# Optimization experiments

Hardware: AMD Instinct MI355X
Metric: run time of the kernel (lower is better)

Reference implementation:

```python
import jax, jax.numpy as jnp
import numpy as np

EPS = 1e-12


def _phi(e):
    # e: [C, L] -> pairwise euclidean distances [C, C], diagonal zeroed
    sq = jnp.sum(e * e, axis=1)                      # [C]
    prod = e @ e.T                                   # [C, C]
    d2 = sq[:, None] + sq[None, :] - 2.0 * prod
    d = jnp.sqrt(jnp.clip(d2, EPS, None))
    C = e.shape[0]
    return d * (1.0 - jnp.eye(C, dtype=e.dtype))


def setup_inputs() -> dict:
    key = jax.random.key(0)
    k1, k2, k3 = jax.random.split(key, 3)
    N, C, L = 64, 512, 256
    le_student = jax.random.normal(k1, (N, C, L), dtype=jnp.float32)
    le_teacher = jax.random.normal(k2, (N, C, L), dtype=jnp.float32)
    targets = jax.random.randint(k3, (N, C), 0, 2, dtype=jnp.int32)
    return {"le_student": le_student, "le_teacher": le_teacher, "targets": targets}


def reference(le_student, le_teacher, targets):
    N, C, L = le_student.shape
    m = targets.astype(le_student.dtype)             # [N, C] 0/1 mask
    es = le_student * m[:, :, None]                  # zero out negative rows
    et = le_teacher * m[:, :, None]

    Ds = jax.vmap(_phi)(es)                          # [N, C, C]
    Dt = jax.vmap(_phi)(et)                          # [N, C, C]

    eye = jnp.eye(C, dtype=m.dtype)
    pm = m[:, :, None] * m[:, None, :]               # pairs of positive rows
    offdiag = pm * (1.0 - eye)                       # off-diagonal positive pairs

    npos = jnp.sum(m, axis=1)                        # [N]
    cnt = npos * (npos - 1.0)                        # entries with d > 0 in submatrix
    valid = npos > 1.0
    safe_cnt = jnp.maximum(cnt, 1.0)

    mean_s = jnp.sum(Ds * offdiag, axis=(1, 2)) / safe_cnt
    mean_t = jax.lax.stop_gradient(jnp.sum(Dt * offdiag, axis=(1, 2)) / safe_cnt)
    mean_s = jnp.where(valid, mean_s, 1.0)
    mean_t = jnp.where(valid, mean_t, 1.0)

    d = Ds / mean_s[:, None, None]
    td = jax.lax.stop_gradient(Dt / mean_t[:, None, None])

    diff = d - td
    adiff = jnp.abs(diff)
    huber = jnp.where(adiff < 1.0, 0.5 * diff * diff, adiff - 0.5)

    per = jnp.sum(huber * pm, axis=(1, 2)) / jnp.maximum(npos, 1.0)
    return jnp.sum(jnp.where(valid, per, 0.0))
```

## Files before the change

kernel.cpp:

```cpp
#include <hip/hip_runtime.h>
#include <hip/hip_bf16.h>
#include <hip/hip_fp16.h>
#include <math.h>

#define NB 64
#define CC 512
#define LL 256

typedef __attribute__((ext_vector_type(4))) float floatx4;
typedef __attribute__((ext_vector_type(8))) short short8;

static __device__ __forceinline__ unsigned f2bf2(float x, float y) {
    __hip_bfloat162 h = __float22bfloat162_rn(make_float2(x, y));
    union { __hip_bfloat162 h; unsigned u; } c; c.h = h;
    return c.u;
}
static __device__ __forceinline__ unsigned short f2h(float x) {
    __half h = __float2half_rn(x);
    union { __half h; unsigned short u; } c; c.h = h;
    return c.u;
}
static __device__ __forceinline__ float h2f(unsigned u) {
    union { unsigned short u; __half h; } c; c.u = (unsigned short)u;
    return __half2float(c.h);
}

__global__ __launch_bounds__(256) void prep_kernel(
    const int* __restrict__ targets,
    int* __restrict__ idx, int* __restrict__ npos,
    float* __restrict__ sumS, float* __restrict__ sumT, float* __restrict__ out)
{
    const int n = blockIdx.x, tid = threadIdx.x;
    __shared__ int s_cnt[8], s_off[8];
    const int w = tid >> 6, lane = tid & 63;
    const int* tg = targets + n * CC;
    const bool p0 = tg[tid] != 0;
    const bool p1 = tg[tid + 256] != 0;
    const unsigned long long m0 = __ballot(p0);
    const unsigned long long m1 = __ballot(p1);
    if (lane == 0) { s_cnt[w] = __popcll(m0); s_cnt[4 + w] = __popcll(m1); }
    __syncthreads();
    if (tid == 0) {
        int a = 0;
        for (int i = 0; i < 8; ++i) { s_off[i] = a; a += s_cnt[i]; }
        npos[n] = a;
        sumS[n] = 0.0f; sumT[n] = 0.0f;
        if (n == 0) out[0] = 0.0f;
    }
    __syncthreads();
    const unsigned long long below = (1ull << lane) - 1ull;
    if (p0) idx[n * CC + s_off[w] + __popcll(m0 & below)] = tid;
    if (p1) idx[n * CC + s_off[4 + w] + __popcll(m1 & below)] = tid + 256;
}

static __device__ __forceinline__ bool decode_tile(int t, int u, int& tI, int& tJ) {
    if (t >= (u * (u + 1)) >> 1) return false;
    tI = 0;
    while (t >= u - tI) { t -= u - tI; ++tI; }
    tJ = tI + t;
    return true;
}

__global__ __launch_bounds__(256) void dist_kernel(
    const float* __restrict__ S, const float* __restrict__ T,
    const int* __restrict__ idx, const int* __restrict__ npos,
    float* __restrict__ sumS, float* __restrict__ sumT,
    unsigned short* __restrict__ Ds, unsigned short* __restrict__ Dt)
{
    const int bx = blockIdx.x;
    const int n = bx & (NB - 1);
    const int q = bx >> 6;
    const int mat = q & 1, t = q >> 1;
    const int np = npos[n];
    if (np < 2) return;
    int tI, tJ;
    if (!decode_tile(t, (np + 63) >> 6, tI, tJ)) return;
    const bool diag = (tI == tJ);

    __shared__ __align__(16) unsigned short lds[2][2][64][40];
    __shared__ float s_norm[2][64];
    __shared__ float red[4];

    const int tid = threadIdx.x;
    const int w = tid >> 6, lane = tid & 63;

    const float* P = (mat ? T : S) + (size_t)n * CC * LL;
    unsigned short* Dout = (mat ? Dt : Ds) + (((size_t)t * NB + n) << 12);
    float* sumP = mat ? sumT : sumS;

    const int srow = w * 32 + (lane >> 1);
    const int half = lane & 1;
    const bool stager = diag ? (srow < 64) : true;
    const int ab = srow >> 6, rloc = srow & 63;
    const int gk = (ab ? tJ : tI) * 64 + rloc;
    const int row = idx[n * CC + ((gk < np) ? gk : 0)];
    const char* rp = (const char*)P + (size_t)row * (LL * 4) + half * 64;

    float4 pre[4];
    float nsum = 0.0f;
    if (stager) {
        #pragma unroll
        for (int i = 0; i < 4; ++i) pre[i] = *(const float4*)(rp + i * 16);
    }

    const int m16 = lane & 15, quad = lane >> 4;
    const int bufB = diag ? 0 : 1;
    const int wrow = w * 16;

    floatx4 acc[4];
    #pragma unroll
    for (int c = 0; c < 4; ++c) { acc[c][0] = 0; acc[c][1] = 0; acc[c][2] = 0; acc[c][3] = 0; }

    for (int kk = 0; kk < 8; ++kk) {
        const int pb = kk & 1;
        if (stager) {
            #pragma unroll
            for (int i = 0; i < 4; ++i)
                nsum += pre[i].x * pre[i].x + pre[i].y * pre[i].y +
                        pre[i].z * pre[i].z + pre[i].w * pre[i].w;
            unsigned short* dst = &lds[ab][pb][rloc][half * 16];
            *(uint2*)(dst + 0)  = make_uint2(f2bf2(pre[0].x, pre[0].y), f2bf2(pre[0].z, pre[0].w));
            *(uint2*)(dst + 4)  = make_uint2(f2bf2(pre[1].x, pre[1].y), f2bf2(pre[1].z, pre[1].w));
            *(uint2*)(dst + 8)  = make_uint2(f2bf2(pre[2].x, pre[2].y), f2bf2(pre[2].z, pre[2].w));
            *(uint2*)(dst + 12) = make_uint2(f2bf2(pre[3].x, pre[3].y), f2bf2(pre[3].z, pre[3].w));
        }
        __syncthreads();
        if (stager && kk < 7) {
            #pragma unroll
            for (int i = 0; i < 4; ++i)
                pre[i] = *(const float4*)(rp + (kk + 1) * 128 + i * 16);
        }
        const short8 a = *(const short8*)&lds[0][pb][wrow + m16][quad * 8];
        #pragma unroll
        for (int c = 0; c < 4; ++c) {
            const short8 b = *(const short8*)&lds[bufB][pb][c * 16 + m16][quad * 8];
            acc[c] = __builtin_amdgcn_mfma_f32_16x16x32_bf16(a, b, acc[c], 0, 0, 0);
        }
    }

    if (stager) {
        const float v = nsum + __shfl_xor(nsum, 1);
        if (half == 0) s_norm[ab][rloc] = v;
    }
    __syncthreads();

    float l0 = 0.0f;
    #pragma unroll
    for (int c = 0; c < 4; ++c) {
        const int colL = c * 16 + m16;
        const int gj = tJ * 64 + colL;
        const float nB = s_norm[bufB][colL];
        #pragma unroll
        for (int r = 0; r < 4; ++r) {
            const int rowL = wrow + quad * 4 + r;
            const int gi = tI * 64 + rowL;
            const float d = sqrtf(fmaxf(s_norm[0][rowL] + nB - 2.0f * acc[c][r], 1e-12f));
            if (gi < np && gj < np && gi != gj) l0 += d;
            Dout[rowL * 64 + colL] = f2h(d);
        }
    }

    #pragma unroll
    for (int o = 32; o; o >>= 1) l0 += __shfl_down(l0, o);
    if (lane == 0) red[w] = l0;
    __syncthreads();
    if (tid == 0) {
        const float wgt = diag ? 1.0f : 2.0f;
        atomicAdd(sumP + n, wgt * (red[0] + red[1] + red[2] + red[3]));
    }
}

__global__ __launch_bounds__(256) void huber_kernel(
    const unsigned short* __restrict__ Ds, const unsigned short* __restrict__ Dt,
    const int* __restrict__ npos,
    const float* __restrict__ sumS, const float* __restrict__ sumT,
    float* __restrict__ out)
{
    const int bx = blockIdx.x;
    const int n = bx & (NB - 1), t = bx >> 6;
    const int np = npos[n];
    if (np < 2) return;
    int tI, tJ;
    if (!decode_tile(t, (np + 63) >> 6, tI, tJ)) return;

    const float cnt = (float)np * (float)(np - 1);
    const float inv_ms = cnt / sumS[n];
    const float inv_mt = cnt / sumT[n];

    const size_t slot = ((size_t)t * NB + n) << 12;
    const uint4* ps = (const uint4*)(Ds + slot);
    const uint4* pt = (const uint4*)(Dt + slot);
    const int tid = threadIdx.x;

    float h = 0.0f;
    #pragma unroll
    for (int it = 0; it < 2; ++it) {
        const int g = it * 256 + tid;
        const uint4 a = ps[g];
        const uint4 b = pt[g];
        const unsigned aw[4] = { a.x, a.y, a.z, a.w };
        const unsigned bw[4] = { b.x, b.y, b.z, b.w };
        const int e0 = g * 8;
        #pragma unroll
        for (int k = 0; k < 8; ++k) {
            const int e = e0 + k;
            const int gi = tI * 64 + (e >> 6);
            const int gj = tJ * 64 + (e & 63);
            if (gi < np && gj < np && gi != gj) {
                const unsigned wa = aw[k >> 1], wb = bw[k >> 1];
                const float ds = h2f((k & 1) ? (wa >> 16) : (wa & 0xffffu));
                const float dt = h2f((k & 1) ? (wb >> 16) : (wb & 0xffffu));
                const float diff = ds * inv_ms - dt * inv_mt;
                const float ad = fabsf(diff);
                h += (ad < 1.0f) ? 0.5f * diff * diff : ad - 0.5f;
            }
        }
    }

    #pragma unroll
    for (int o = 32; o; o >>= 1) h += __shfl_down(h, o);
    __shared__ float red[4];
    const int w = tid >> 6, lane = tid & 63;
    if (lane == 0) red[w] = h;
    __syncthreads();
    if (tid == 0) {
        const float wgt = (tI == tJ) ? 1.0f : 2.0f;
        atomicAdd(out, wgt * (red[0] + red[1] + red[2] + red[3]) / (float)np);
    }
}

extern "C" void kernel_launch(void* const* d_in, const int* in_sizes, int n_in,
                              void* d_out, int out_size, void* d_ws, size_t ws_size,
                              hipStream_t stream) {
    const float* S = (const float*)d_in[0];
    const float* T = (const float*)d_in[1];
    const int* targets = (const int*)d_in[2];
    float* out = (float*)d_out;

    char* p = (char*)d_ws;
    int* idx = (int*)p;        p += (size_t)NB * CC * 4;
    int* npos = (int*)p;       p += NB * 4;
    float* sumS = (float*)p;   p += NB * 4;
    float* sumT = (float*)p;   p += NB * 4;
    p = (char*)(((size_t)p + 255) & ~(size_t)255);
    unsigned short* Ds = (unsigned short*)p;   p += (size_t)36 * NB * 4096 * 2;
    unsigned short* Dt = (unsigned short*)p;

    prep_kernel<<<NB, 256, 0, stream>>>(targets, idx, npos, sumS, sumT, out);
    dist_kernel<<<72 * NB, 256, 0, stream>>>(S, T, idx, npos, sumS, sumT, Ds, Dt);
    huber_kernel<<<36 * NB, 256, 0, stream>>>(Ds, Dt, npos, sumS, sumT, out);
}
```

Measured before the change: 124.8 us.

## Fuse Huber pass into distance kernel via last-block-per-batch tail, deepen prefetch

Removes the separate huber kernel launch. Each distance block increments a per-batch counter, and the last block to finish for a batch reads all of that batch's Ds/Dt tiles and accumulates the Huber loss. It also double-buffers the global prefetch registers so loads run two K-steps ahead. The trade is a serialized tail: one block walks up to 36 tiles alone per batch, and threadfence/atomic ordering adds overhead to every block.

After: 393.7 us. +215.5%, slower.

```diff
diff --git a/kernel.cpp b/kernel.cpp
--- a/kernel.cpp
+++ b/kernel.cpp
@@ -28,7 +28,8 @@
 __global__ __launch_bounds__(256) void prep_kernel(
     const int* __restrict__ targets,
     int* __restrict__ idx, int* __restrict__ npos,
-    float* __restrict__ sumS, float* __restrict__ sumT, float* __restrict__ out)
+    float* __restrict__ sumS, float* __restrict__ sumT,
+    int* __restrict__ count, float* __restrict__ out)
 {
     const int n = blockIdx.x, tid = threadIdx.x;
     __shared__ int s_cnt[8], s_off[8];
@@ -45,6 +46,7 @@
         for (int i = 0; i < 8; ++i) { s_off[i] = a; a += s_cnt[i]; }
         npos[n] = a;
         sumS[n] = 0.0f; sumT[n] = 0.0f;
+        count[n * 16] = 0;
         if (n == 0) out[0] = 0.0f;
     }
     __syncthreads();
@@ -65,7 +67,9 @@
     const float* __restrict__ S, const float* __restrict__ T,
     const int* __restrict__ idx, const int* __restrict__ npos,
     float* __restrict__ sumS, float* __restrict__ sumT,
-    unsigned short* __restrict__ Ds, unsigned short* __restrict__ Dt)
+    int* __restrict__ count,
+    unsigned short* __restrict__ Ds, unsigned short* __restrict__ Dt,
+    float* __restrict__ out)
 {
     const int bx = blockIdx.x;
     const int n = bx & (NB - 1);
@@ -73,13 +77,16 @@
     const int mat = q & 1, t = q >> 1;
     const int np = npos[n];
     if (np < 2) return;
+    const int u = (np + 63) >> 6;
+    const int ntiles = (u * (u + 1)) >> 1;
     int tI, tJ;
-    if (!decode_tile(t, (np + 63) >> 6, tI, tJ)) return;
+    if (!decode_tile(t, u, tI, tJ)) return;
     const bool diag = (tI == tJ);
 
     __shared__ __align__(16) unsigned short lds[2][2][64][40];
     __shared__ float s_norm[2][64];
     __shared__ float red[4];
+    __shared__ int s_tail;
 
     const int tid = threadIdx.x;
     const int w = tid >> 6, lane = tid & 63;
@@ -96,11 +103,13 @@
     const int row = idx[n * CC + ((gk < np) ? gk : 0)];
     const char* rp = (const char*)P + (size_t)row * (LL * 4) + half * 64;
 
-    float4 pre[4];
+    float4 pre[2][4];
     float nsum = 0.0f;
     if (stager) {
         #pragma unroll
-        for (int i = 0; i < 4; ++i) pre[i] = *(const float4*)(rp + i * 16);
+        for (int i = 0; i < 4; ++i) pre[0][i] = *(const float4*)(rp + i * 16);
+        #pragma unroll
+        for (int i = 0; i < 4; ++i) pre[1][i] = *(const float4*)(rp + 128 + i * 16);
     }
 
     const int m16 = lane & 15, quad = lane >> 4;
@@ -116,19 +125,19 @@
         if (stager) {
             #pragma unroll
             for (int i = 0; i < 4; ++i)
-                nsum += pre[i].x * pre[i].x + pre[i].y * pre[i].y +
-                        pre[i].z * pre[i].z + pre[i].w * pre[i].w;
+                nsum += pre[pb][i].x * pre[pb][i].x + pre[pb][i].y * pre[pb][i].y +
+                        pre[pb][i].z * pre[pb][i].z + pre[pb][i].w * pre[pb][i].w;
             unsigned short* dst = &lds[ab][pb][rloc][half * 16];
-            *(uint2*)(dst + 0)  = make_uint2(f2bf2(pre[0].x, pre[0].y), f2bf2(pre[0].z, pre[0].w));
-            *(uint2*)(dst + 4)  = make_uint2(f2bf2(pre[1].x, pre[1].y), f2bf2(pre[1].z, pre[1].w));
-            *(uint2*)(dst + 8)  = make_uint2(f2bf2(pre[2].x, pre[2].y), f2bf2(pre[2].z, pre[2].w));
-            *(uint2*)(dst + 12) = make_uint2(f2bf2(pre[3].x, pre[3].y), f2bf2(pre[3].z, pre[3].w));
+            *(uint2*)(dst + 0)  = make_uint2(f2bf2(pre[pb][0].x, pre[pb][0].y), f2bf2(pre[pb][0].z, pre[pb][0].w));
+            *(uint2*)(dst + 4)  = make_uint2(f2bf2(pre[pb][1].x, pre[pb][1].y), f2bf2(pre[pb][1].z, pre[pb][1].w));
+            *(uint2*)(dst + 8)  = make_uint2(f2bf2(pre[pb][2].x, pre[pb][2].y), f2bf2(pre[pb][2].z, pre[pb][2].w));
+            *(uint2*)(dst + 12) = make_uint2(f2bf2(pre[pb][3].x, pre[pb][3].y), f2bf2(pre[pb][3].z, pre[pb][3].w));
         }
         __syncthreads();
-        if (stager && kk < 7) {
+        if (stager && kk < 6) {
             #pragma unroll
             for (int i = 0; i < 4; ++i)
-                pre[i] = *(const float4*)(rp + (kk + 1) * 128 + i * 16);
+                pre[pb][i] = *(const float4*)(rp + (kk + 2) * 128 + i * 16);
         }
         const short8 a = *(const short8*)&lds[0][pb][wrow + m16][quad * 8];
         #pragma unroll
@@ -164,69 +173,69 @@
     for (int o = 32; o; o >>= 1) l0 += __shfl_down(l0, o);
     if (lane == 0) red[w] = l0;
     __syncthreads();
+
+    __threadfence();
+    __syncthreads();
     if (tid == 0) {
         const float wgt = diag ? 1.0f : 2.0f;
         atomicAdd(sumP + n, wgt * (red[0] + red[1] + red[2] + red[3]));
-    }
-}
-
-__global__ __launch_bounds__(256) void huber_kernel(
-    const unsigned short* __restrict__ Ds, const unsigned short* __restrict__ Dt,
-    const int* __restrict__ npos,
-    const float* __restrict__ sumS, const float* __restrict__ sumT,
-    float* __restrict__ out)
-{
-    const int bx = blockIdx.x;
-    const int n = bx & (NB - 1), t = bx >> 6;
-    const int np = npos[n];
-    if (np < 2) return;
-    int tI, tJ;
-    if (!decode_tile(t, (np + 63) >> 6, tI, tJ)) return;
-
-    const float cnt = (float)np * (float)(np - 1);
-    const float inv_ms = cnt / sumS[n];
-    const float inv_mt = cnt / sumT[n];
-
-    const size_t slot = ((size_t)t * NB + n) << 12;
-    const uint4* ps = (const uint4*)(Ds + slot);
-    const uint4* pt = (const uint4*)(Dt + slot);
-    const int tid = threadIdx.x;
+        __threadfence();
+        const int old = __hip_atomic_fetch_add(&count[n * 16], 1, __ATOMIC_ACQ_REL,
+                                               __HIP_MEMORY_SCOPE_AGENT);
+        s_tail = (old == 2 * ntiles - 1);
+    }
+    __syncthreads();
+    if (!s_tail) return;
+    __threadfence();
+
+    const float cp = (float)np * (float)(np - 1);
+    const float inv_ms = cp / __hip_atomic_load(&sumS[n], __ATOMIC_RELAXED,
+                                                __HIP_MEMORY_SCOPE_AGENT);
+    const float inv_mt = cp / __hip_atomic_load(&sumT[n], __ATOMIC_RELAXED,
+                                                __HIP_MEMORY_SCOPE_AGENT);
 
     float h = 0.0f;
-    #pragma unroll
-    for (int it = 0; it < 2; ++it) {
-        const int g = it * 256 + tid;
-        const uint4 a = ps[g];
-        const uint4 b = pt[g];
-        const unsigned aw[4] = { a.x, a.y, a.z, a.w };
-        const unsigned bw[4] = { b.x, b.y, b.z, b.w };
-        const int e0 = g * 8;
-        #pragma unroll
-        for (int k = 0; k < 8; ++k) {
-            const int e = e0 + k;
-            const int gi = tI * 64 + (e >> 6);
-            const int gj = tJ * 64 + (e & 63);
-            if (gi < np && gj < np && gi != gj) {
-                const unsigned wa = aw[k >> 1], wb = bw[k >> 1];
-                const float ds = h2f((k & 1) ? (wa >> 16) : (wa & 0xffffu));
-                const float dt = h2f((k & 1) ? (wb >> 16) : (wb & 0xffffu));
-                const float diff = ds * inv_ms - dt * inv_mt;
-                const float ad = fabsf(diff);
-                h += (ad < 1.0f) ? 0.5f * diff * diff : ad - 0.5f;
+    int ti = 0, tj = 0;
+    for (int tt = 0; tt < ntiles; ++tt) {
+        const size_t slot = ((size_t)tt * NB + n) << 12;
+        const uint4* ps = (const uint4*)(Ds + slot);
+        const uint4* pt = (const uint4*)(Dt + slot);
+        const float wgt = (ti == tj) ? 1.0f : 2.0f;
+        float hp = 0.0f;
+        #pragma unroll
+        for (int it = 0; it < 2; ++it) {
+            const int g = it * 256 + tid;
+            const uint4 a = ps[g];
+            const uint4 b = pt[g];
+            const unsigned aw[4] = { a.x, a.y, a.z, a.w };
+            const unsigned bw[4] = { b.x, b.y, b.z, b.w };
+            const int e0 = g * 8;
+            #pragma unroll
+            for (int k = 0; k < 8; ++k) {
+                const int e = e0 + k;
+                const int gi = ti * 64 + (e >> 6);
+                const int gj = tj * 64 + (e & 63);
+                if (gi < np && gj < np && gi != gj) {
+                    const unsigned wa = aw[k >> 1], wb = bw[k >> 1];
+                    const float ds = h2f((k & 1) ? (wa >> 16) : (wa & 0xffffu));
+                    const float dt = h2f((k & 1) ? (wb >> 16) : (wb & 0xffffu));
+                    const float diff = ds * inv_ms - dt * inv_mt;
+                    const float ad = fabsf(diff);
+                    hp += (ad < 1.0f) ? 0.5f * diff * diff : ad - 0.5f;
+                }
             }
         }
+        h += wgt * hp;
+        ++tj;
+        if (tj == u) { ++ti; tj = ti; }
     }
 
     #pragma unroll
     for (int o = 32; o; o >>= 1) h += __shfl_down(h, o);
-    __shared__ float red[4];
-    const int w = tid >> 6, lane = tid & 63;
     if (lane == 0) red[w] = h;
     __syncthreads();
-    if (tid == 0) {
-        const float wgt = (tI == tJ) ? 1.0f : 2.0f;
-        atomicAdd(out, wgt * (red[0] + red[1] + red[2] + red[3]) / (float)np);
-    }
+    if (tid == 0)
+        atomicAdd(out, (red[0] + red[1] + red[2] + red[3]) / (float)np);
 }
 
 extern "C" void kernel_launch(void* const* d_in, const int* in_sizes, int n_in,
@@ -242,11 +251,12 @@
     int* npos = (int*)p;       p += NB * 4;
     float* sumS = (float*)p;   p += NB * 4;
     float* sumT = (float*)p;   p += NB * 4;
+    int* count = (int*)p;      p += NB * 16 * 4;
     p = (char*)(((size_t)p + 255) & ~(size_t)255);
     unsigned short* Ds = (unsigned short*)p;   p += (size_t)36 * NB * 4096 * 2;
     unsigned short* Dt = (unsigned short*)p;
 
-    prep_kernel<<<NB, 256, 0, stream>>>(targets, idx, npos, sumS, sumT, out);
-    dist_kernel<<<72 * NB, 256, 0, stream>>>(S, T, idx, npos, sumS, sumT, Ds, Dt);
-    huber_kernel<<<36 * NB, 256, 0, stream>>>(Ds, Dt, npos, sumS, sumT, out);
-}
+    prep_kernel<<<NB, 256, 0, stream>>>(targets, idx, npos, sumS, sumT, count, out);
+    dist_kernel<<<72 * NB, 256, 0, stream>>>(S, T, idx, npos, sumS, sumT, count,
+                                             Ds, Dt, out);
+}
```
